# Kernel optimization log

Hardware: AMD Instinct MI355X
Metric: run time of the kernel (lower is better)

Reference implementation:

```python
import jax, jax.numpy as jnp
import numpy as np

B, S, H = 2, 2048, 2048
E, I, SH = 8, 768, 5632
TOP_K = 2


def setup_inputs() -> dict:
    key = jax.random.key(0)
    ks = jax.random.split(key, 8)
    sc = lambda *shape: 1.0 / np.sqrt(shape[-2] if len(shape) > 1 else 1.0)
    return {
        "hidden_states": jax.random.normal(ks[0], (B, S, H), jnp.float32),
        "router_w": jax.random.normal(ks[1], (H, E), jnp.float32) * (1.0 / np.sqrt(H)),
        "expert_gate_up_w": jax.random.normal(ks[2], (E, H, 2 * I), jnp.float32) * (1.0 / np.sqrt(H)),
        "expert_down_w": jax.random.normal(ks[3], (E, I, H), jnp.float32) * (1.0 / np.sqrt(I)),
        "shared_gate_w": jax.random.normal(ks[4], (H, SH), jnp.float32) * (1.0 / np.sqrt(H)),
        "shared_up_w": jax.random.normal(ks[5], (H, SH), jnp.float32) * (1.0 / np.sqrt(H)),
        "shared_down_w": jax.random.normal(ks[6], (SH, H), jnp.float32) * (1.0 / np.sqrt(SH)),
        "shared_expert_gate_w": jax.random.normal(ks[7], (H, 1), jnp.float32) * (1.0 / np.sqrt(H)),
    }


def reference(hidden_states, router_w, expert_gate_up_w, expert_down_w,
              shared_gate_w, shared_up_w, shared_down_w, shared_expert_gate_w):
    b, s, h = hidden_states.shape
    x = hidden_states.reshape(-1, h)  # [T, H]

    # Shared expert (SwiGLU) gated by sigmoid scalar gate per token.
    gate = jax.nn.silu((x @ shared_gate_w).astype(jnp.float32)).astype(x.dtype)
    shared_out = (gate * (x @ shared_up_w)) @ shared_down_w  # [T, H]
    shared_out = jax.nn.sigmoid(x @ shared_expert_gate_w) * shared_out

    # Router: softmax -> top-k -> renormalize -> dense routing weights [E, T].
    router_logits = x @ router_w  # [T, E]
    router_probs = jax.nn.softmax(router_logits, axis=-1)
    top_p, top_i = jax.lax.top_k(router_probs, TOP_K)  # [T, k]
    top_p = top_p / jnp.sum(top_p, axis=-1, keepdims=True)
    one_hot = jax.nn.one_hot(top_i, E, dtype=top_p.dtype)  # [T, k, E]
    routing_full = jnp.sum(one_hot * top_p[..., None], axis=1)  # [T, E]
    routing_full = routing_full.T.astype(x.dtype)  # [E, T]

    # Dense per-expert SwiGLU over all tokens (as in source einsums).
    gate_up = jnp.einsum('th,ehm->etm', x, expert_gate_up_w)  # [E, T, 2I]
    g, u = jnp.split(gate_up, 2, axis=-1)
    g = jax.nn.silu(g.astype(jnp.float32)).astype(x.dtype)
    expert_out = jnp.einsum('eti,eih->eth', u * g, expert_down_w)  # [E, T, H]

    expert_contribution = jnp.sum(expert_out * routing_full[:, :, None], axis=0)  # [T, H]
    out = (expert_contribution + shared_out).reshape(b, s, h)
    return out, router_logits
```

## Files before the change

### kernel.cpp

```cpp
#include <hip/hip_runtime.h>
#include <hip/hip_bf16.h>
#include <stdint.h>

#define DEVFN static __device__ __forceinline__

typedef __attribute__((ext_vector_type(8))) short bf16x8;
typedef __attribute__((ext_vector_type(4))) float f32x4;
typedef unsigned short u16;
typedef unsigned int u32;
typedef unsigned long long u64;

DEVFN u16 f2bf(float f) {
    union { float f; u32 u; } v; v.f = f;
    u32 r = v.u + 0x7FFFu + ((v.u >> 16) & 1u);
    return (u16)(r >> 16);
}

DEVFN void g2l16(const void* g, void* l) {
    __builtin_amdgcn_global_load_lds(
        (const __attribute__((address_space(1))) u32*)g,
        (__attribute__((address_space(3))) u32*)l, 16, 0, 0);
}

DEVFN void hbar() {
    __asm__ __volatile__("" ::: "memory");
    __builtin_amdgcn_s_barrier();
    __asm__ __volatile__("" ::: "memory");
}
DEVFN void vm4() { asm volatile("s_waitcnt vmcnt(4)" ::: "memory"); }
DEVFN void vm0() { asm volatile("s_waitcnt vmcnt(0)" ::: "memory"); }

__global__ __launch_bounds__(512, 2) void gemm8_swiglu_k(
    const u16* __restrict__ A, const u16* __restrict__ Bg,
    const u16* __restrict__ Bu, u16* __restrict__ out,
    int K, int nx, int ldc)
{
    extern __shared__ char smraw[];
    char* smA = smraw;
    char* smB = smraw + 65536;

    const int tid = threadIdx.x;
    const int lane = tid & 63, wv = tid >> 6;
    const int wm = wv >> 2, wn = wv & 3;
    const int l15 = lane & 15, kg = lane >> 4;

    const int nwg = gridDim.x;
    const int id = (blockIdx.x & 7) * (nwg >> 3) + (blockIdx.x >> 3);
    const int m0 = (id / nx) * 256, n0 = (id % nx) * 128;

    const u16* Ap  = A  + (long)m0 * K;
    const u16* Bgp = Bg + (long)n0 * K;
    const u16* Bup = Bu + (long)n0 * K;

    f32x4 accg[8][2], accu[8][2];
#pragma unroll
    for (int i = 0; i < 8; ++i)
#pragma unroll
        for (int j = 0; j < 2; ++j) {
            accg[i][j] = f32x4{0.f, 0.f, 0.f, 0.f};
            accu[i][j] = f32x4{0.f, 0.f, 0.f, 0.f};
        }

    auto stA = [&](int kt, int hh, int buf) {
        const u16* src = Ap + ((long)hh * 128) * K + kt * 64;
        char* dst = smA + buf * 32768 + hh * 16384;
#pragma unroll
        for (int i = 0; i < 2; ++i) {
            int slot = i * 512 + tid;
            int row = slot >> 3, ch = slot & 7;
            g2l16(src + (long)row * K + ((ch ^ (row & 7)) << 3), dst + slot * 16);
        }
    };
    auto stB = [&](int kt, int hh, int buf) {
        const u16* src = (hh ? Bup : Bgp) + kt * 64;
        char* dst = smB + buf * 32768 + hh * 16384;
#pragma unroll
        for (int i = 0; i < 2; ++i) {
            int slot = i * 512 + tid;
            int row = slot >> 3, ch = slot & 7;
            g2l16(src + (long)row * K + ((ch ^ (row & 7)) << 3), dst + slot * 16);
        }
    };
    auto frag = [&](const char* base, int r, int c) -> bf16x8 {
        return *(const __attribute__((address_space(3))) bf16x8*)
            (base + r * 128 + ((c ^ (r & 7)) << 4));
    };

    stA(0, 0, 0); stA(0, 1, 0);
    stB(0, 0, 0); stB(0, 1, 0);
    stB(1, 0, 1); stB(1, 1, 1);
    vm4();
    hbar();

    const int nk = K >> 6;
    for (int kt = 0; kt < nk; kt += 2) {
        const bool more = (kt + 2) < nk;
#pragma unroll
        for (int h = 0; h < 2; ++h) {
            const char* ab = smA + h * 32768;
            const char* bb = smB + h * 32768;
            bf16x8 bgv[2][2], buv[2][2];
#pragma unroll
            for (int p = 0; p < 4; ++p) {
                if (p == 0) {
#pragma unroll
                    for (int fn = 0; fn < 2; ++fn)
#pragma unroll
                        for (int s = 0; s < 2; ++s) {
                            int rB = wn * 32 + fn * 16 + l15;
                            bgv[fn][s] = frag(bb, rB, s * 4 + kg);
                            buv[fn][s] = frag(bb + 16384, rB, s * 4 + kg);
                        }
                }
                bf16x8 av[2][2];
#pragma unroll
                for (int am = 0; am < 2; ++am)
#pragma unroll
                    for (int s = 0; s < 2; ++s)
                        av[am][s] = frag(ab, wm * 128 + (p * 2 + am) * 16 + l15,
                                         s * 4 + kg);
                if (h == 0) {
                    if (p == 0)      { stA(kt + 1, 0, 1); stA(kt + 1, 1, 1); }
                    else if (p == 1) { if (more) stB(kt + 2, 0, 0); }
                    else if (p == 2) { if (more) stB(kt + 2, 1, 0); }
                    else             { if (more) vm4(); else vm0(); }
                } else {
                    if (more) {
                        if (p == 0)      stA(kt + 2, 0, 0);
                        else if (p == 1) stA(kt + 2, 1, 0);
                        else if (p == 2) stB(kt + 3, 0, 1);
                        else             { stB(kt + 3, 1, 1); vm4(); }
                    }
                }
                hbar();
                __builtin_amdgcn_sched_barrier(0);
                __builtin_amdgcn_s_setprio(1);
#pragma unroll
                for (int am = 0; am < 2; ++am)
#pragma unroll
                    for (int s = 0; s < 2; ++s)
#pragma unroll
                        for (int fn = 0; fn < 2; ++fn) {
                            accg[p * 2 + am][fn] = __builtin_amdgcn_mfma_f32_16x16x32_bf16(
                                av[am][s], bgv[fn][s], accg[p * 2 + am][fn], 0, 0, 0);
                            accu[p * 2 + am][fn] = __builtin_amdgcn_mfma_f32_16x16x32_bf16(
                                av[am][s], buv[fn][s], accu[p * 2 + am][fn], 0, 0, 0);
                        }
                __builtin_amdgcn_s_setprio(0);
                __builtin_amdgcn_sched_barrier(0);
                hbar();
            }
        }
    }

    const int lq = lane >> 4;
#pragma unroll
    for (int fm = 0; fm < 8; ++fm)
#pragma unroll
        for (int j = 0; j < 4; ++j) {
            int row = m0 + wm * 128 + fm * 16 + lq * 4 + j;
#pragma unroll
            for (int fn = 0; fn < 2; ++fn) {
                int col = n0 + wn * 32 + fn * 16 + l15;
                float g = accg[fm][fn][j], u = accu[fm][fn][j];
                float s = g * (1.f / (1.f + __expf(-g))) * u;
                out[(long)row * ldc + col] = f2bf(s);
            }
        }
}

template<int NSLOT>
DEVFN void stage(const u16* __restrict__ src, int ldk, u16* lds, int tid) {
#pragma unroll
    for (int i = 0; i < NSLOT / 256; ++i) {
        int slot = i * 256 + tid;
        int row = slot >> 2, chunk = slot & 3;
        int kg = chunk ^ ((row >> 1) & 3);
        g2l16(src + (long)row * ldk + kg * 8, lds + slot * 8);
    }
}

DEVFN bf16x8 ld_frag(const u16* lds, int row, int kg) {
    int chunk = kg ^ ((row >> 1) & 3);
    const u16* p = lds + row * 32 + chunk * 8;
    return *(const __attribute__((address_space(3))) bf16x8*)p;
}

__global__ __launch_bounds__(256) void gemm_down_k(
    const u16* __restrict__ A, const u16* __restrict__ B,
    float* __restrict__ C, const float* __restrict__ gvec,
    int K, int ldc)
{
    __shared__ u16 sm[2][8192];
    const int tid = threadIdx.x;
    const int lane = tid & 63, wv = tid >> 6;
    const int wm = wv >> 1, wn = wv & 1;
    const int m0 = blockIdx.y * 128, n0 = blockIdx.x * 128;
    const u16* Ab = A + (long)m0 * K;
    const u16* Bb = B + (long)n0 * K;

    f32x4 acc[4][4];
#pragma unroll
    for (int i = 0; i < 4; ++i)
#pragma unroll
        for (int j = 0; j < 4; ++j) acc[i][j] = f32x4{0.f, 0.f, 0.f, 0.f};

    stage<512>(Ab, K, &sm[0][0], tid);
    stage<512>(Bb, K, &sm[0][4096], tid);

    const int nk = K >> 5;
    for (int kt = 0; kt < nk; ++kt) {
        const int cur = kt & 1;
        __syncthreads();
        if (kt + 1 < nk) {
            stage<512>(Ab + (kt + 1) * 32, K, &sm[cur ^ 1][0], tid);
            stage<512>(Bb + (kt + 1) * 32, K, &sm[cur ^ 1][4096], tid);
        }
        const int l15 = lane & 15, kg = lane >> 4;
        bf16x8 av[4], bv[4];
#pragma unroll
        for (int f = 0; f < 4; ++f) {
            av[f] = ld_frag(&sm[cur][0],    wm * 64 + f * 16 + l15, kg);
            bv[f] = ld_frag(&sm[cur][4096], wn * 64 + f * 16 + l15, kg);
        }
#pragma unroll
        for (int fm = 0; fm < 4; ++fm)
#pragma unroll
            for (int fn = 0; fn < 4; ++fn)
                acc[fm][fn] = __builtin_amdgcn_mfma_f32_16x16x32_bf16(
                    av[fm], bv[fn], acc[fm][fn], 0, 0, 0);
    }

    const int l15 = lane & 15, lq = lane >> 4;
#pragma unroll
    for (int fm = 0; fm < 4; ++fm) {
#pragma unroll
        for (int j = 0; j < 4; ++j) {
            int row = m0 + wm * 64 + fm * 16 + lq * 4 + j;
            float gmul = gvec[row];
#pragma unroll
            for (int fn = 0; fn < 4; ++fn) {
                int col = n0 + wn * 64 + fn * 16 + l15;
                C[(long)row * ldc + col] = acc[fm][fn][j] * gmul;
            }
        }
    }
}

__global__ __launch_bounds__(256) void gemm_swiglu_moe_k(
    const u16* __restrict__ xb, const u16* __restrict__ Beg,
    const u16* __restrict__ Beu, const int* __restrict__ tok,
    const int* __restrict__ cntp, u16* __restrict__ eact,
    int K, int I_, int cap)
{
    const int e = blockIdx.z;
    const int m0 = blockIdx.y * 128;
    if (m0 >= cntp[e]) return;
    const int n0 = blockIdx.x * 64;

    __shared__ u16 sm[2][8192];
    const int tid = threadIdx.x;
    const int lane = tid & 63, wv = tid >> 6;
    const int wm = wv >> 1, wn = wv & 1;

    const int rA0 = tid >> 2, rA1 = 64 + (tid >> 2);
    const int* tseg = tok + (long)e * cap + m0;
    const long t0 = tseg[rA0], t1 = tseg[rA1];
    const int kg0 = (tid & 3) ^ ((rA0 >> 1) & 3);
    const int kg1 = (tid & 3) ^ ((rA1 >> 1) & 3);
    const u16* pa0 = xb + t0 * K + kg0 * 8;
    const u16* pa1 = xb + t1 * K + kg1 * 8;

    const u16* Bgb = Beg + ((long)e * I_ + n0) * K;
    const u16* Bub = Beu + ((long)e * I_ + n0) * K;

    f32x4 ag[4][2], au[4][2];
#pragma unroll
    for (int i = 0; i < 4; ++i)
#pragma unroll
        for (int j = 0; j < 2; ++j) {
            ag[i][j] = f32x4{0.f, 0.f, 0.f, 0.f};
            au[i][j] = f32x4{0.f, 0.f, 0.f, 0.f};
        }

    g2l16(pa0, &sm[0][(long)tid * 8]);
    g2l16(pa1, &sm[0][(long)(256 + tid) * 8]);
    stage<256>(Bgb, K, &sm[0][4096], tid);
    stage<256>(Bub, K, &sm[0][6144], tid);

    const int nk = K >> 5;
    for (int kt = 0; kt < nk; ++kt) {
        const int cur = kt & 1;
        __syncthreads();
        if (kt + 1 < nk) {
            g2l16(pa0 + (kt + 1) * 32, &sm[cur ^ 1][(long)tid * 8]);
            g2l16(pa1 + (kt + 1) * 32, &sm[cur ^ 1][(long)(256 + tid) * 8]);
            stage<256>(Bgb + (kt + 1) * 32, K, &sm[cur ^ 1][4096], tid);
            stage<256>(Bub + (kt + 1) * 32, K, &sm[cur ^ 1][6144], tid);
        }
        const int l15 = lane & 15, kg = lane >> 4;
        bf16x8 av[4], gv[2], uv[2];
#pragma unroll
        for (int f = 0; f < 4; ++f)
            av[f] = ld_frag(&sm[cur][0], wm * 64 + f * 16 + l15, kg);
#pragma unroll
        for (int f = 0; f < 2; ++f) {
            gv[f] = ld_frag(&sm[cur][4096], wn * 32 + f * 16 + l15, kg);
            uv[f] = ld_frag(&sm[cur][6144], wn * 32 + f * 16 + l15, kg);
        }
#pragma unroll
        for (int fm = 0; fm < 4; ++fm)
#pragma unroll
            for (int fn = 0; fn < 2; ++fn) {
                ag[fm][fn] = __builtin_amdgcn_mfma_f32_16x16x32_bf16(
                    av[fm], gv[fn], ag[fm][fn], 0, 0, 0);
                au[fm][fn] = __builtin_amdgcn_mfma_f32_16x16x32_bf16(
                    av[fm], uv[fn], au[fm][fn], 0, 0, 0);
            }
    }

    const int l15 = lane & 15, lq = lane >> 4;
#pragma unroll
    for (int fm = 0; fm < 4; ++fm) {
#pragma unroll
        for (int j = 0; j < 4; ++j) {
            long row = (long)e * cap + m0 + wm * 64 + fm * 16 + lq * 4 + j;
#pragma unroll
            for (int fn = 0; fn < 2; ++fn) {
                int col = n0 + wn * 32 + fn * 16 + l15;
                float g = ag[fm][fn][j], u = au[fm][fn][j];
                float s = g * (1.f / (1.f + __expf(-g))) * u;
                eact[row * I_ + col] = f2bf(s);
            }
        }
    }
}

__global__ __launch_bounds__(256) void gemm_down_moe_k(
    const u16* __restrict__ eact, const u16* __restrict__ Bed,
    float* __restrict__ out, const int* __restrict__ tok,
    const float* __restrict__ wrow, const int* __restrict__ cntp,
    int K, int ldc, int cap)
{
    const int e = blockIdx.z;
    const int m0 = blockIdx.y * 128;
    if (m0 >= cntp[e]) return;
    const int n0 = blockIdx.x * 128;

    __shared__ u16 sm[2][8192];
    const int tid = threadIdx.x;
    const int lane = tid & 63, wv = tid >> 6;
    const int wm = wv >> 1, wn = wv & 1;
    const u16* Ab = eact + ((long)e * cap + m0) * K;
    const u16* Bb = Bed + (long)e * ldc * K + (long)n0 * K;

    f32x4 acc[4][4];
#pragma unroll
    for (int i = 0; i < 4; ++i)
#pragma unroll
        for (int j = 0; j < 4; ++j) acc[i][j] = f32x4{0.f, 0.f, 0.f, 0.f};

    stage<512>(Ab, K, &sm[0][0], tid);
    stage<512>(Bb, K, &sm[0][4096], tid);

    const int nk = K >> 5;
    for (int kt = 0; kt < nk; ++kt) {
        const int cur = kt & 1;
        __syncthreads();
        if (kt + 1 < nk) {
            stage<512>(Ab + (kt + 1) * 32, K, &sm[cur ^ 1][0], tid);
            stage<512>(Bb + (kt + 1) * 32, K, &sm[cur ^ 1][4096], tid);
        }
        const int l15 = lane & 15, kg = lane >> 4;
        bf16x8 av[4], bv[4];
#pragma unroll
        for (int f = 0; f < 4; ++f) {
            av[f] = ld_frag(&sm[cur][0],    wm * 64 + f * 16 + l15, kg);
            bv[f] = ld_frag(&sm[cur][4096], wn * 64 + f * 16 + l15, kg);
        }
#pragma unroll
        for (int fm = 0; fm < 4; ++fm)
#pragma unroll
            for (int fn = 0; fn < 4; ++fn)
                acc[fm][fn] = __builtin_amdgcn_mfma_f32_16x16x32_bf16(
                    av[fm], bv[fn], acc[fm][fn], 0, 0, 0);
    }

    const int l15 = lane & 15, lq = lane >> 4;
#pragma unroll
    for (int fm = 0; fm < 4; ++fm) {
#pragma unroll
        for (int j = 0; j < 4; ++j) {
            long crow = (long)e * cap + m0 + wm * 64 + fm * 16 + lq * 4 + j;
            float w = wrow[crow];
            if (w != 0.f) {
                long t = tok[crow];
#pragma unroll
                for (int fn = 0; fn < 4; ++fn) {
                    int col = n0 + wn * 64 + fn * 16 + l15;
                    atomicAdd(out + t * ldc + col, acc[fm][fn][j] * w);
                }
            }
        }
    }
}

__global__ __launch_bounds__(256) void router_k(
    const float* __restrict__ x, const float* __restrict__ rw,
    const float* __restrict__ sgw, float* __restrict__ logits,
    int2* __restrict__ te, float2* __restrict__ tw,
    float* __restrict__ sig, int T, int H)
{
    const int tid = threadIdx.x, lane = tid & 63, wv = tid >> 6;
    const int t = blockIdx.x * 4 + wv;
    const float* xr = x + (long)t * H;
    float acc[8] = {0, 0, 0, 0, 0, 0, 0, 0};
    float as = 0.f;
    for (int h = lane; h < H; h += 64) {
        float xv = xr[h];
        const float* r = rw + h * 8;
#pragma unroll
        for (int e = 0; e < 8; ++e) acc[e] += xv * r[e];
        as += xv * sgw[h];
    }
#pragma unroll
    for (int off = 32; off; off >>= 1) {
#pragma unroll
        for (int e = 0; e < 8; ++e) acc[e] += __shfl_xor(acc[e], off);
        as += __shfl_xor(as, off);
    }
    if (lane == 0) {
        float mx = acc[0];
#pragma unroll
        for (int e = 1; e < 8; ++e) mx = fmaxf(mx, acc[e]);
        float p[8], sum = 0.f;
#pragma unroll
        for (int e = 0; e < 8; ++e) { p[e] = expf(acc[e] - mx); sum += p[e]; }
        int i1 = 0;
#pragma unroll
        for (int e = 1; e < 8; ++e) if (p[e] > p[i1]) i1 = e;
        int i2 = (i1 == 0) ? 1 : 0;
#pragma unroll
        for (int e = 0; e < 8; ++e) if (e != i1 && p[e] > p[i2]) i2 = e;
        float den = p[i1] + p[i2];
        te[t] = make_int2(i1, i2);
        tw[t] = make_float2(p[i1] / den, p[i2] / den);
#pragma unroll
        for (int e = 0; e < 8; ++e) logits[(long)t * 8 + e] = acc[e];
        sig[t] = 1.f / (1.f + expf(-as));
    }
}

__global__ __launch_bounds__(256) void compact_k(
    const int2* __restrict__ te, const float2* __restrict__ tw,
    int* __restrict__ tok, float* __restrict__ wrow,
    int* __restrict__ cntp, int T, int cap)
{
    const int e = blockIdx.x;
    const int tid = threadIdx.x, lane = tid & 63, wv = tid >> 6;
    __shared__ int wtot[4];
    int cnt = 0;
    for (int c0 = 0; c0 < T; c0 += 256) {
        int t = c0 + tid;
        int2 ids = te[t];
        float2 ws = tw[t];
        float w = (ids.x == e) ? ws.x : ((ids.y == e) ? ws.y : -1.f);
        bool sel = (w >= 0.f);
        u64 b = __ballot(sel);
        int rln = __popcll(b & ((1ull << lane) - 1ull));
        if (lane == 0) wtot[wv] = __popcll(b);
        __syncthreads();
        int rank = rln, tot = 0;
#pragma unroll
        for (int k = 0; k < 4; ++k) { if (k < wv) rank += wtot[k]; tot += wtot[k]; }
        if (sel) {
            int pos = cnt + rank;
            if (pos < cap) {
                tok[(long)e * cap + pos] = t;
                wrow[(long)e * cap + pos] = w;
            }
        }
        cnt += tot;
        __syncthreads();
    }
    if (cnt > cap) cnt = cap;
    int cp = (cnt + 127) & ~127;
    for (int p = cnt + tid; p < cp; p += 256) {
        tok[(long)e * cap + p] = 0;
        wrow[(long)e * cap + p] = 0.f;
    }
    if (tid == 0) cntp[e] = cp;
}

__global__ __launch_bounds__(256) void transpose_k(
    const float* __restrict__ src0, long src_zstr, int src_ld,
    u16* __restrict__ dst0, long dst_zstr, int dst_ld)
{
    __shared__ float tile[32][33];
    const float* src = src0 + (long)blockIdx.z * src_zstr;
    u16* dst = dst0 + (long)blockIdx.z * dst_zstr;
    int r0 = blockIdx.y * 32, c0 = blockIdx.x * 32;
    int tx = threadIdx.x, ty = threadIdx.y;
#pragma unroll
    for (int k = 0; k < 4; ++k)
        tile[ty + 8 * k][tx] = src[(long)(r0 + ty + 8 * k) * src_ld + c0 + tx];
    __syncthreads();
#pragma unroll
    for (int k = 0; k < 4; ++k)
        dst[(long)(c0 + ty + 8 * k) * dst_ld + r0 + tx] = f2bf(tile[tx][ty + 8 * k]);
}

__global__ __launch_bounds__(256) void cvt_x_k(const float* __restrict__ x,
                                               u16* __restrict__ xb)
{
    long i = ((long)blockIdx.x * 256 + threadIdx.x) * 4;
    float4 v = *(const float4*)(x + i);
    union { u16 s[4]; uint2 v2; } o;
    o.s[0] = f2bf(v.x); o.s[1] = f2bf(v.y); o.s[2] = f2bf(v.z); o.s[3] = f2bf(v.w);
    *(uint2*)(xb + i) = o.v2;
}

extern "C" void kernel_launch(void* const* d_in, const int* in_sizes, int n_in,
                              void* d_out, int out_size, void* d_ws, size_t ws_size,
                              hipStream_t stream) {
    (void)in_sizes; (void)n_in; (void)out_size; (void)ws_size;
    const int Hd = 2048, E = 8, I = 768, SH = 5632, T = 4096, CAP = 2048;

    const float* x    = (const float*)d_in[0];
    const float* rw   = (const float*)d_in[1];
    const float* egu  = (const float*)d_in[2];
    const float* edw  = (const float*)d_in[3];
    const float* sgw  = (const float*)d_in[4];
    const float* suw  = (const float*)d_in[5];
    const float* sdw  = (const float*)d_in[6];
    const float* segw = (const float*)d_in[7];
    float* out = (float*)d_out;
    float* logits = out + (size_t)T * Hd;

    char* wsp = (char*)d_ws;
    size_t off = 0;
    auto alloc = [&](size_t bytes) {
        void* p = wsp + off; off += (bytes + 255) & ~(size_t)255; return p;
    };
    u16* xb   = (u16*)alloc((size_t)T * Hd * 2);
    u16* Bgs  = (u16*)alloc((size_t)SH * Hd * 2);
    u16* Bus  = (u16*)alloc((size_t)SH * Hd * 2);
    u16* Bds  = (u16*)alloc((size_t)Hd * SH * 2);
    u16* Beg  = (u16*)alloc((size_t)E * I * Hd * 2);
    u16* Beu  = (u16*)alloc((size_t)E * I * Hd * 2);
    u16* Bed  = (u16*)alloc((size_t)E * Hd * I * 2);
    u16* hs   = (u16*)alloc((size_t)T * SH * 2);
    u16* eact = (u16*)alloc((size_t)E * CAP * I * 2);
    int2*   te   = (int2*)alloc((size_t)T * 8);
    float2* tw   = (float2*)alloc((size_t)T * 8);
    int*    tok  = (int*)alloc((size_t)E * CAP * 4);
    float*  wrow = (float*)alloc((size_t)E * CAP * 4);
    int*    cntp = (int*)alloc(64);
    float*  sig  = (float*)alloc((size_t)T * 4);

    hipFuncSetAttribute((const void*)gemm8_swiglu_k,
                        hipFuncAttributeMaxDynamicSharedMemorySize, 131072);

    dim3 tb(32, 8);
    cvt_x_k<<<(T * Hd) / 1024, 256, 0, stream>>>(x, xb);
    router_k<<<T / 4, 256, 0, stream>>>(x, rw, segw, logits, te, tw, sig, T, Hd);
    compact_k<<<E, 256, 0, stream>>>(te, tw, tok, wrow, cntp, T, CAP);

    transpose_k<<<dim3(SH / 32, Hd / 32), tb, 0, stream>>>(sgw, 0, SH, Bgs, 0, Hd);
    transpose_k<<<dim3(SH / 32, Hd / 32), tb, 0, stream>>>(suw, 0, SH, Bus, 0, Hd);
    transpose_k<<<dim3(Hd / 32, SH / 32), tb, 0, stream>>>(sdw, 0, Hd, Bds, 0, SH);
    transpose_k<<<dim3(I / 32, Hd / 32, E), tb, 0, stream>>>(
        egu, (long)Hd * 2 * I, 2 * I, Beg, (long)I * Hd, Hd);
    transpose_k<<<dim3(I / 32, Hd / 32, E), tb, 0, stream>>>(
        egu + I, (long)Hd * 2 * I, 2 * I, Beu, (long)I * Hd, Hd);
    transpose_k<<<dim3(Hd / 32, I / 32, E), tb, 0, stream>>>(
        edw, (long)I * Hd, Hd, Bed, (long)Hd * I, I);

    gemm8_swiglu_k<<<dim3((SH / 128) * (T / 256)), 512, 131072, stream>>>(
        xb, Bgs, Bus, hs, Hd, SH / 128, SH);
    gemm_down_k<<<dim3(Hd / 128, T / 128), 256, 0, stream>>>(
        hs, Bds, out, sig, SH, Hd);
    gemm_swiglu_moe_k<<<dim3(I / 64, CAP / 128, E), 256, 0, stream>>>(
        xb, Beg, Beu, tok, cntp, eact, Hd, I, CAP);
    gemm_down_moe_k<<<dim3(Hd / 128, CAP / 128, E), 256, 0, stream>>>(
        eact, Bed, out, tok, wrow, cntp, I, Hd, CAP);
}
```

Before: 612.3 us.

## Software-pipeline LDS fragment reads in shared GEMM and add 8-wave down GEMM

The shared-expert gate/up GEMM's main loop now runs as 8 phases. Each phase prefetches the next phase's A/B fragments from LDS into double-buffered registers while the MFMAs for the current phase run, with one barrier per phase instead of two, and global-to-LDS loads are interleaved with relaxed vmcnt waits. The shared down-projection GEMM is replaced by a new 512-thread, 256x128-tile kernel that uses the same pipelined scheme, replacing the 256-thread 128x128 kernel with single-stage 32-wide K steps. The aim is to hide LDS latency and cut barrier overhead, at the cost of more registers and a tricky wait/barrier ordering that could race if miscounted.

```diff
diff --git a/kernel.cpp b/kernel.cpp
--- a/kernel.cpp
+++ b/kernel.cpp
@@ -22,13 +22,17 @@
         (__attribute__((address_space(3))) u32*)l, 16, 0, 0);
 }
 
-DEVFN void hbar() {
-    __asm__ __volatile__("" ::: "memory");
+DEVFN void vmw0() { asm volatile("s_waitcnt vmcnt(0)" ::: "memory"); }
+DEVFN void vmw2() { asm volatile("s_waitcnt vmcnt(2)" ::: "memory"); }
+DEVFN void vmw4() { asm volatile("s_waitcnt vmcnt(4)" ::: "memory"); }
+DEVFN void vmw6() { asm volatile("s_waitcnt vmcnt(6)" ::: "memory"); }
+DEVFN void vmw8() { asm volatile("s_waitcnt vmcnt(8)" ::: "memory"); }
+DEVFN void pbar() {
+    __builtin_amdgcn_sched_barrier(0);
     __builtin_amdgcn_s_barrier();
-    __asm__ __volatile__("" ::: "memory");
-}
-DEVFN void vm4() { asm volatile("s_waitcnt vmcnt(4)" ::: "memory"); }
-DEVFN void vm0() { asm volatile("s_waitcnt vmcnt(0)" ::: "memory"); }
+}
+
+#define MFMA16(a, b, c) __builtin_amdgcn_mfma_f32_16x16x32_bf16(a, b, c, 0, 0, 0)
 
 __global__ __launch_bounds__(512, 2) void gemm8_swiglu_k(
     const u16* __restrict__ A, const u16* __restrict__ Bg,
@@ -86,70 +90,67 @@
             (base + r * 128 + ((c ^ (r & 7)) << 4));
     };
 
-    stA(0, 0, 0); stA(0, 1, 0);
-    stB(0, 0, 0); stB(0, 1, 0);
-    stB(1, 0, 1); stB(1, 1, 1);
-    vm4();
-    hbar();
+    bf16x8 af[2][4];
+    bf16x8 bgf[2][2], buf2[2][2];
+
+    auto rdA = [&](int par, int h, int s, int fmh) {
+#pragma unroll
+        for (int i = 0; i < 4; ++i)
+            af[par][i] = frag(smA + h * 32768,
+                              wm * 128 + fmh * 64 + i * 16 + l15, s * 4 + kg);
+    };
+    auto rdB = [&](int set, int h, int s) {
+#pragma unroll
+        for (int fn = 0; fn < 2; ++fn) {
+            bgf[set][fn] = frag(smB + h * 32768,
+                                wn * 32 + fn * 16 + l15, s * 4 + kg);
+            buf2[set][fn] = frag(smB + h * 32768 + 16384,
+                                 wn * 32 + fn * 16 + l15, s * 4 + kg);
+        }
+    };
+
+    stA(0, 0, 0); stA(0, 1, 0); stB(0, 0, 0); stB(0, 1, 0);
+    stA(1, 0, 1); stA(1, 1, 1); stB(1, 0, 1); stB(1, 1, 1);
+    vmw8();
+    __builtin_amdgcn_s_barrier();
+    rdA(0, 0, 0, 0);
+    rdB(0, 0, 0);
 
     const int nk = K >> 6;
     for (int kt = 0; kt < nk; kt += 2) {
         const bool more = (kt + 2) < nk;
 #pragma unroll
-        for (int h = 0; h < 2; ++h) {
-            const char* ab = smA + h * 32768;
-            const char* bb = smB + h * 32768;
-            bf16x8 bgv[2][2], buv[2][2];
-#pragma unroll
-            for (int p = 0; p < 4; ++p) {
-                if (p == 0) {
-#pragma unroll
-                    for (int fn = 0; fn < 2; ++fn)
-#pragma unroll
-                        for (int s = 0; s < 2; ++s) {
-                            int rB = wn * 32 + fn * 16 + l15;
-                            bgv[fn][s] = frag(bb, rB, s * 4 + kg);
-                            buv[fn][s] = frag(bb + 16384, rB, s * 4 + kg);
-                        }
+        for (int p = 0; p < 8; ++p) {
+            if (p < 7) {
+                const int tp = p + 1;
+                rdA(tp & 1, tp >> 2, (tp >> 1) & 1, tp & 1);
+                if ((tp & 1) == 0) rdB((tp >> 1) & 1, tp >> 2, (tp >> 1) & 1);
+            } else if (more) {
+                rdA(0, 0, 0, 0);
+                rdB(0, 0, 0);
+            }
+            if (more) {
+                if (p == 3)      stB(kt + 2, 0, 0);
+                else if (p == 4) { stB(kt + 2, 1, 0); stA(kt + 2, 0, 0); }
+                else if (p == 5) stA(kt + 2, 1, 0);
+                else if (p == 6) stB(kt + 3, 0, 1);
+                else if (p == 7) { stB(kt + 3, 1, 1); stA(kt + 3, 0, 1); stA(kt + 3, 1, 1); }
+            }
+            if (p == 2) vmw0();
+            if (p == 6 && more) vmw2();
+            pbar();
+            __builtin_amdgcn_s_setprio(1);
+            const int fb = p & 1, sb = (p >> 1) & 1;
+#pragma unroll
+            for (int i = 0; i < 4; ++i)
+#pragma unroll
+                for (int fn = 0; fn < 2; ++fn) {
+                    accg[fb * 4 + i][fn] = MFMA16(af[fb][i], bgf[sb][fn],
+                                                  accg[fb * 4 + i][fn]);
+                    accu[fb * 4 + i][fn] = MFMA16(af[fb][i], buf2[sb][fn],
+                                                  accu[fb * 4 + i][fn]);
                 }
-                bf16x8 av[2][2];
-#pragma unroll
-                for (int am = 0; am < 2; ++am)
-#pragma unroll
-                    for (int s = 0; s < 2; ++s)
-                        av[am][s] = frag(ab, wm * 128 + (p * 2 + am) * 16 + l15,
-                                         s * 4 + kg);
-                if (h == 0) {
-                    if (p == 0)      { stA(kt + 1, 0, 1); stA(kt + 1, 1, 1); }
-                    else if (p == 1) { if (more) stB(kt + 2, 0, 0); }
-                    else if (p == 2) { if (more) stB(kt + 2, 1, 0); }
-                    else             { if (more) vm4(); else vm0(); }
-                } else {
-                    if (more) {
-                        if (p == 0)      stA(kt + 2, 0, 0);
-                        else if (p == 1) stA(kt + 2, 1, 0);
-                        else if (p == 2) stB(kt + 3, 0, 1);
-                        else             { stB(kt + 3, 1, 1); vm4(); }
-                    }
-                }
-                hbar();
-                __builtin_amdgcn_sched_barrier(0);
-                __builtin_amdgcn_s_setprio(1);
-#pragma unroll
-                for (int am = 0; am < 2; ++am)
-#pragma unroll
-                    for (int s = 0; s < 2; ++s)
-#pragma unroll
-                        for (int fn = 0; fn < 2; ++fn) {
-                            accg[p * 2 + am][fn] = __builtin_amdgcn_mfma_f32_16x16x32_bf16(
-                                av[am][s], bgv[fn][s], accg[p * 2 + am][fn], 0, 0, 0);
-                            accu[p * 2 + am][fn] = __builtin_amdgcn_mfma_f32_16x16x32_bf16(
-                                av[am][s], buv[fn][s], accu[p * 2 + am][fn], 0, 0, 0);
-                        }
-                __builtin_amdgcn_s_setprio(0);
-                __builtin_amdgcn_sched_barrier(0);
-                hbar();
-            }
+            __builtin_amdgcn_s_setprio(0);
         }
     }
 
@@ -169,6 +170,130 @@
         }
 }
 
+__global__ __launch_bounds__(512, 2) void gemm8_down_k(
+    const u16* __restrict__ A, const u16* __restrict__ B,
+    float* __restrict__ C, const float* __restrict__ gvec,
+    int K, int nx, int ldc)
+{
+    extern __shared__ char smraw[];
+    char* smA = smraw;
+    char* smB = smraw + 65536;
+
+    const int tid = threadIdx.x;
+    const int lane = tid & 63, wv = tid >> 6;
+    const int wm = wv >> 2, wn = wv & 3;
+    const int l15 = lane & 15, kg = lane >> 4;
+
+    const int nwg = gridDim.x;
+    const int id = (blockIdx.x & 7) * (nwg >> 3) + (blockIdx.x >> 3);
+    const int m0 = (id / nx) * 256, n0 = (id % nx) * 128;
+
+    const u16* Ap = A + (long)m0 * K;
+    const u16* Bp = B + (long)n0 * K;
+
+    f32x4 acc[8][2];
+#pragma unroll
+    for (int i = 0; i < 8; ++i)
+#pragma unroll
+        for (int j = 0; j < 2; ++j) acc[i][j] = f32x4{0.f, 0.f, 0.f, 0.f};
+
+    auto stA = [&](int kt, int hh, int buf) {
+        const u16* src = Ap + ((long)hh * 128) * K + kt * 64;
+        char* dst = smA + buf * 32768 + hh * 16384;
+#pragma unroll
+        for (int i = 0; i < 2; ++i) {
+            int slot = i * 512 + tid;
+            int row = slot >> 3, ch = slot & 7;
+            g2l16(src + (long)row * K + ((ch ^ (row & 7)) << 3), dst + slot * 16);
+        }
+    };
+    auto stB1 = [&](int kt, int buf) {
+        const u16* src = Bp + kt * 64;
+        char* dst = smB + buf * 16384;
+#pragma unroll
+        for (int i = 0; i < 2; ++i) {
+            int slot = i * 512 + tid;
+            int row = slot >> 3, ch = slot & 7;
+            g2l16(src + (long)row * K + ((ch ^ (row & 7)) << 3), dst + slot * 16);
+        }
+    };
+    auto frag = [&](const char* base, int r, int c) -> bf16x8 {
+        return *(const __attribute__((address_space(3))) bf16x8*)
+            (base + r * 128 + ((c ^ (r & 7)) << 4));
+    };
+
+    bf16x8 af[2][4], bf_[2][2];
+
+    auto rdA = [&](int par, int h, int s, int fmh) {
+#pragma unroll
+        for (int i = 0; i < 4; ++i)
+            af[par][i] = frag(smA + h * 32768,
+                              wm * 128 + fmh * 64 + i * 16 + l15, s * 4 + kg);
+    };
+    auto rdB = [&](int set, int h, int s) {
+#pragma unroll
+        for (int fn = 0; fn < 2; ++fn)
+            bf_[set][fn] = frag(smB + h * 16384,
+                                wn * 32 + fn * 16 + l15, s * 4 + kg);
+    };
+
+    stA(0, 0, 0); stA(0, 1, 0); stB1(0, 0);
+    stA(1, 0, 1); stA(1, 1, 1); stB1(1, 1);
+    vmw6();
+    __builtin_amdgcn_s_barrier();
+    rdA(0, 0, 0, 0);
+    rdB(0, 0, 0);
+
+    const int nk = K >> 6;
+    for (int kt = 0; kt < nk; kt += 2) {
+        const bool more = (kt + 2) < nk;
+#pragma unroll
+        for (int p = 0; p < 8; ++p) {
+            if (p < 7) {
+                const int tp = p + 1;
+                rdA(tp & 1, tp >> 2, (tp >> 1) & 1, tp & 1);
+                if ((tp & 1) == 0) rdB((tp >> 1) & 1, tp >> 2, (tp >> 1) & 1);
+            } else if (more) {
+                rdA(0, 0, 0, 0);
+                rdB(0, 0, 0);
+            }
+            if (more) {
+                if (p == 3)      stB1(kt + 2, 0);
+                else if (p == 4) stA(kt + 2, 0, 0);
+                else if (p == 5) stA(kt + 2, 1, 0);
+                else if (p == 6) stB1(kt + 3, 1);
+                else if (p == 7) { stA(kt + 3, 0, 1); stA(kt + 3, 1, 1); }
+            }
+            if (p == 2) vmw0();
+            if (p == 6 && more) vmw2();
+            pbar();
+            __builtin_amdgcn_s_setprio(1);
+            const int fb = p & 1, sb = (p >> 1) & 1;
+#pragma unroll
+            for (int i = 0; i < 4; ++i)
+#pragma unroll
+                for (int fn = 0; fn < 2; ++fn)
+                    acc[fb * 4 + i][fn] = MFMA16(af[fb][i], bf_[sb][fn],
+                                                 acc[fb * 4 + i][fn]);
+            __builtin_amdgcn_s_setprio(0);
+        }
+    }
+
+    const int lq = lane >> 4;
+#pragma unroll
+    for (int fm = 0; fm < 8; ++fm)
+#pragma unroll
+        for (int j = 0; j < 4; ++j) {
+            int row = m0 + wm * 128 + fm * 16 + lq * 4 + j;
+            float gmul = gvec[row];
+#pragma unroll
+            for (int fn = 0; fn < 2; ++fn) {
+                int col = n0 + wn * 32 + fn * 16 + l15;
+                C[(long)row * ldc + col] = acc[fm][fn][j] * gmul;
+            }
+        }
+}
+
 template<int NSLOT>
 DEVFN void stage(const u16* __restrict__ src, int ldk, u16* lds, int tid) {
 #pragma unroll
@@ -184,67 +309,6 @@
     int chunk = kg ^ ((row >> 1) & 3);
     const u16* p = lds + row * 32 + chunk * 8;
     return *(const __attribute__((address_space(3))) bf16x8*)p;
-}
-
-__global__ __launch_bounds__(256) void gemm_down_k(
-    const u16* __restrict__ A, const u16* __restrict__ B,
-    float* __restrict__ C, const float* __restrict__ gvec,
-    int K, int ldc)
-{
-    __shared__ u16 sm[2][8192];
-    const int tid = threadIdx.x;
-    const int lane = tid & 63, wv = tid >> 6;
-    const int wm = wv >> 1, wn = wv & 1;
-    const int m0 = blockIdx.y * 128, n0 = blockIdx.x * 128;
-    const u16* Ab = A + (long)m0 * K;
-    const u16* Bb = B + (long)n0 * K;
-
-    f32x4 acc[4][4];
-#pragma unroll
-    for (int i = 0; i < 4; ++i)
-#pragma unroll
-        for (int j = 0; j < 4; ++j) acc[i][j] = f32x4{0.f, 0.f, 0.f, 0.f};
-
-    stage<512>(Ab, K, &sm[0][0], tid);
-    stage<512>(Bb, K, &sm[0][4096], tid);
-
-    const int nk = K >> 5;
-    for (int kt = 0; kt < nk; ++kt) {
-        const int cur = kt & 1;
-        __syncthreads();
-        if (kt + 1 < nk) {
-            stage<512>(Ab + (kt + 1) * 32, K, &sm[cur ^ 1][0], tid);
-            stage<512>(Bb + (kt + 1) * 32, K, &sm[cur ^ 1][4096], tid);
-        }
-        const int l15 = lane & 15, kg = lane >> 4;
-        bf16x8 av[4], bv[4];
-#pragma unroll
-        for (int f = 0; f < 4; ++f) {
-            av[f] = ld_frag(&sm[cur][0],    wm * 64 + f * 16 + l15, kg);
-            bv[f] = ld_frag(&sm[cur][4096], wn * 64 + f * 16 + l15, kg);
-        }
-#pragma unroll
-        for (int fm = 0; fm < 4; ++fm)
-#pragma unroll
-            for (int fn = 0; fn < 4; ++fn)
-                acc[fm][fn] = __builtin_amdgcn_mfma_f32_16x16x32_bf16(
-                    av[fm], bv[fn], acc[fm][fn], 0, 0, 0);
-    }
-
-    const int l15 = lane & 15, lq = lane >> 4;
-#pragma unroll
-    for (int fm = 0; fm < 4; ++fm) {
-#pragma unroll
-        for (int j = 0; j < 4; ++j) {
-            int row = m0 + wm * 64 + fm * 16 + lq * 4 + j;
-            float gmul = gvec[row];
-#pragma unroll
-            for (int fn = 0; fn < 4; ++fn) {
-                int col = n0 + wn * 64 + fn * 16 + l15;
-                C[(long)row * ldc + col] = acc[fm][fn][j] * gmul;
-            }
-        }
-    }
 }
 
 __global__ __launch_bounds__(256) void gemm_swiglu_moe_k(
@@ -312,10 +376,8 @@
         for (int fm = 0; fm < 4; ++fm)
 #pragma unroll
             for (int fn = 0; fn < 2; ++fn) {
-                ag[fm][fn] = __builtin_amdgcn_mfma_f32_16x16x32_bf16(
-                    av[fm], gv[fn], ag[fm][fn], 0, 0, 0);
-                au[fm][fn] = __builtin_amdgcn_mfma_f32_16x16x32_bf16(
-                    av[fm], uv[fn], au[fm][fn], 0, 0, 0);
+                ag[fm][fn] = MFMA16(av[fm], gv[fn], ag[fm][fn]);
+                au[fm][fn] = MFMA16(av[fm], uv[fn], au[fm][fn]);
             }
     }
 
@@ -382,8 +444,7 @@
         for (int fm = 0; fm < 4; ++fm)
 #pragma unroll
             for (int fn = 0; fn < 4; ++fn)
-                acc[fm][fn] = __builtin_amdgcn_mfma_f32_16x16x32_bf16(
-                    av[fm], bv[fn], acc[fm][fn], 0, 0, 0);
+                acc[fm][fn] = MFMA16(av[fm], bv[fn], acc[fm][fn]);
     }
 
     const int l15 = lane & 15, lq = lane >> 4;
@@ -560,6 +621,8 @@
 
     hipFuncSetAttribute((const void*)gemm8_swiglu_k,
                         hipFuncAttributeMaxDynamicSharedMemorySize, 131072);
+    hipFuncSetAttribute((const void*)gemm8_down_k,
+                        hipFuncAttributeMaxDynamicSharedMemorySize, 98304);
 
     dim3 tb(32, 8);
     cvt_x_k<<<(T * Hd) / 1024, 256, 0, stream>>>(x, xb);
@@ -578,8 +641,8 @@
 
     gemm8_swiglu_k<<<dim3((SH / 128) * (T / 256)), 512, 131072, stream>>>(
         xb, Bgs, Bus, hs, Hd, SH / 128, SH);
-    gemm_down_k<<<dim3(Hd / 128, T / 128), 256, 0, stream>>>(
-        hs, Bds, out, sig, SH, Hd);
+    gemm8_down_k<<<dim3((Hd / 128) * (T / 256)), 512, 98304, stream>>>(
+        hs, Bds, out, sig, SH, Hd / 128, Hd);
     gemm_swiglu_moe_k<<<dim3(I / 64, CAP / 128, E), 256, 0, stream>>>(
         xb, Beg, Beu, tok, cntp, eact, Hd, I, CAP);
     gemm_down_moe_k<<<dim3(Hd / 128, CAP / 128, E), 256, 0, stream>>>(
```

New measurement: 1.169 ms. 90.9% more time.

## Port routed-expert gate/up GEMM to the 256x128 pipelined 8-wave kernel

Applied to the files above, without the earlier changes.

Replaces the simple double-buffered 128x64 MoE gate/up kernel with a version of the shared-expert 512-thread kernel. It uses 256x128 tiles, gathered token rows, a multi-stage global-to-LDS pipeline and fused SwiGLU. Per-expert token counts are now padded to multiples of 256, capped at capacity, so the larger tiles line up with the padding. The intent is more data reuse per tile and better overlap of loads with MFMA work. The cost is more padded rows per expert and fewer blocks in flight.

```diff
diff --git a/kernel.cpp b/kernel.cpp
--- a/kernel.cpp
+++ b/kernel.cpp
@@ -30,6 +30,8 @@
 DEVFN void vm4() { asm volatile("s_waitcnt vmcnt(4)" ::: "memory"); }
 DEVFN void vm0() { asm volatile("s_waitcnt vmcnt(0)" ::: "memory"); }
 
+#define MFMA16(a, b, c) __builtin_amdgcn_mfma_f32_16x16x32_bf16(a, b, c, 0, 0, 0)
+
 __global__ __launch_bounds__(512, 2) void gemm8_swiglu_k(
     const u16* __restrict__ A, const u16* __restrict__ Bg,
     const u16* __restrict__ Bu, u16* __restrict__ out,
@@ -83,7 +85,7 @@
     };
     auto frag = [&](const char* base, int r, int c) -> bf16x8 {
         return *(const __attribute__((address_space(3))) bf16x8*)
-            (base + r * 128 + ((c ^ (r & 7)) << 4));
+            (base + r * 128 + (((c) ^ (r & 7)) << 4));
     };
 
     stA(0, 0, 0); stA(0, 1, 0);
@@ -141,10 +143,10 @@
                     for (int s = 0; s < 2; ++s)
 #pragma unroll
                         for (int fn = 0; fn < 2; ++fn) {
-                            accg[p * 2 + am][fn] = __builtin_amdgcn_mfma_f32_16x16x32_bf16(
-                                av[am][s], bgv[fn][s], accg[p * 2 + am][fn], 0, 0, 0);
-                            accu[p * 2 + am][fn] = __builtin_amdgcn_mfma_f32_16x16x32_bf16(
-                                av[am][s], buv[fn][s], accu[p * 2 + am][fn], 0, 0, 0);
+                            accg[p * 2 + am][fn] = MFMA16(av[am][s], bgv[fn][s],
+                                                          accg[p * 2 + am][fn]);
+                            accu[p * 2 + am][fn] = MFMA16(av[am][s], buv[fn][s],
+                                                          accu[p * 2 + am][fn]);
                         }
                 __builtin_amdgcn_s_setprio(0);
                 __builtin_amdgcn_sched_barrier(0);
@@ -165,6 +167,151 @@
                 float g = accg[fm][fn][j], u = accu[fm][fn][j];
                 float s = g * (1.f / (1.f + __expf(-g))) * u;
                 out[(long)row * ldc + col] = f2bf(s);
+            }
+        }
+}
+
+__global__ __launch_bounds__(512, 2) void gemm8e_swiglu_k(
+    const u16* __restrict__ xb, const u16* __restrict__ Beg,
+    const u16* __restrict__ Beu, const int* __restrict__ tok,
+    const int* __restrict__ cntp, u16* __restrict__ eact,
+    int K, int ldc, int cap)
+{
+    const int e = blockIdx.z;
+    const int m0 = blockIdx.y * 256;
+    if (m0 >= cntp[e]) return;
+    const int n0 = blockIdx.x * 128;
+
+    extern __shared__ char smraw[];
+    char* smA = smraw;
+    char* smB = smraw + 65536;
+
+    const int tid = threadIdx.x;
+    const int lane = tid & 63, wv = tid >> 6;
+    const int wm = wv >> 2, wn = wv & 3;
+    const int l15 = lane & 15, kg = lane >> 4;
+
+    const int r0 = tid >> 3, ch = tid & 7;
+    const int swz = (ch ^ (r0 & 7)) << 3;
+    const int* tseg = tok + (long)e * cap + m0;
+    const u16* pa00 = xb + (long)tseg[r0] * K + swz;
+    const u16* pa01 = xb + (long)tseg[64 + r0] * K + swz;
+    const u16* pa10 = xb + (long)tseg[128 + r0] * K + swz;
+    const u16* pa11 = xb + (long)tseg[192 + r0] * K + swz;
+
+    const u16* Bgp = Beg + ((long)e * ldc + n0) * K;
+    const u16* Bup = Beu + ((long)e * ldc + n0) * K;
+
+    f32x4 accg[8][2], accu[8][2];
+#pragma unroll
+    for (int i = 0; i < 8; ++i)
+#pragma unroll
+        for (int j = 0; j < 2; ++j) {
+            accg[i][j] = f32x4{0.f, 0.f, 0.f, 0.f};
+            accu[i][j] = f32x4{0.f, 0.f, 0.f, 0.f};
+        }
+
+    auto stA = [&](int kt, int hh, int buf) {
+        char* dst = smA + buf * 32768 + hh * 16384;
+        const u16* p0 = hh ? pa10 : pa00;
+        const u16* p1 = hh ? pa11 : pa01;
+        g2l16(p0 + kt * 64, dst + (long)tid * 16);
+        g2l16(p1 + kt * 64, dst + (long)(512 + tid) * 16);
+    };
+    auto stB = [&](int kt, int hh, int buf) {
+        const u16* src = (hh ? Bup : Bgp) + kt * 64;
+        char* dst = smB + buf * 32768 + hh * 16384;
+#pragma unroll
+        for (int i = 0; i < 2; ++i) {
+            int slot = i * 512 + tid;
+            int row = slot >> 3, c = slot & 7;
+            g2l16(src + (long)row * K + ((c ^ (row & 7)) << 3), dst + slot * 16);
+        }
+    };
+    auto frag = [&](const char* base, int r, int c) -> bf16x8 {
+        return *(const __attribute__((address_space(3))) bf16x8*)
+            (base + r * 128 + (((c) ^ (r & 7)) << 4));
+    };
+
+    stA(0, 0, 0); stA(0, 1, 0);
+    stB(0, 0, 0); stB(0, 1, 0);
+    stB(1, 0, 1); stB(1, 1, 1);
+    vm4();
+    hbar();
+
+    const int nk = K >> 6;
+    for (int kt = 0; kt < nk; kt += 2) {
+        const bool more = (kt + 2) < nk;
+#pragma unroll
+        for (int h = 0; h < 2; ++h) {
+            const char* ab = smA + h * 32768;
+            const char* bb = smB + h * 32768;
+            bf16x8 bgv[2][2], buv[2][2];
+#pragma unroll
+            for (int p = 0; p < 4; ++p) {
+                if (p == 0) {
+#pragma unroll
+                    for (int fn = 0; fn < 2; ++fn)
+#pragma unroll
+                        for (int s = 0; s < 2; ++s) {
+                            int rB = wn * 32 + fn * 16 + l15;
+                            bgv[fn][s] = frag(bb, rB, s * 4 + kg);
+                            buv[fn][s] = frag(bb + 16384, rB, s * 4 + kg);
+                        }
+                }
+                bf16x8 av[2][2];
+#pragma unroll
+                for (int am = 0; am < 2; ++am)
+#pragma unroll
+                    for (int s = 0; s < 2; ++s)
+                        av[am][s] = frag(ab, wm * 128 + (p * 2 + am) * 16 + l15,
+                                         s * 4 + kg);
+                if (h == 0) {
+                    if (p == 0)      { stA(kt + 1, 0, 1); stA(kt + 1, 1, 1); }
+                    else if (p == 1) { if (more) stB(kt + 2, 0, 0); }
+                    else if (p == 2) { if (more) stB(kt + 2, 1, 0); }
+                    else             { if (more) vm4(); else vm0(); }
+                } else {
+                    if (more) {
+                        if (p == 0)      stA(kt + 2, 0, 0);
+                        else if (p == 1) stA(kt + 2, 1, 0);
+                        else if (p == 2) stB(kt + 3, 0, 1);
+                        else             { stB(kt + 3, 1, 1); vm4(); }
+                    }
+                }
+                hbar();
+                __builtin_amdgcn_sched_barrier(0);
+                __builtin_amdgcn_s_setprio(1);
+#pragma unroll
+                for (int am = 0; am < 2; ++am)
+#pragma unroll
+                    for (int s = 0; s < 2; ++s)
+#pragma unroll
+                        for (int fn = 0; fn < 2; ++fn) {
+                            accg[p * 2 + am][fn] = MFMA16(av[am][s], bgv[fn][s],
+                                                          accg[p * 2 + am][fn]);
+                            accu[p * 2 + am][fn] = MFMA16(av[am][s], buv[fn][s],
+                                                          accu[p * 2 + am][fn]);
+                        }
+                __builtin_amdgcn_s_setprio(0);
+                __builtin_amdgcn_sched_barrier(0);
+                hbar();
+            }
+        }
+    }
+
+    const int lq = lane >> 4;
+#pragma unroll
+    for (int fm = 0; fm < 8; ++fm)
+#pragma unroll
+        for (int j = 0; j < 4; ++j) {
+            long row = (long)e * cap + m0 + wm * 128 + fm * 16 + lq * 4 + j;
+#pragma unroll
+            for (int fn = 0; fn < 2; ++fn) {
+                int col = n0 + wn * 32 + fn * 16 + l15;
+                float g = accg[fm][fn][j], u = accu[fm][fn][j];
+                float s = g * (1.f / (1.f + __expf(-g))) * u;
+                eact[row * ldc + col] = f2bf(s);
             }
         }
 }
@@ -227,8 +374,7 @@
         for (int fm = 0; fm < 4; ++fm)
 #pragma unroll
             for (int fn = 0; fn < 4; ++fn)
-                acc[fm][fn] = __builtin_amdgcn_mfma_f32_16x16x32_bf16(
-                    av[fm], bv[fn], acc[fm][fn], 0, 0, 0);
+                acc[fm][fn] = MFMA16(av[fm], bv[fn], acc[fm][fn]);
     }
 
     const int l15 = lane & 15, lq = lane >> 4;
@@ -242,95 +388,6 @@
             for (int fn = 0; fn < 4; ++fn) {
                 int col = n0 + wn * 64 + fn * 16 + l15;
                 C[(long)row * ldc + col] = acc[fm][fn][j] * gmul;
-            }
-        }
-    }
-}
-
-__global__ __launch_bounds__(256) void gemm_swiglu_moe_k(
-    const u16* __restrict__ xb, const u16* __restrict__ Beg,
-    const u16* __restrict__ Beu, const int* __restrict__ tok,
-    const int* __restrict__ cntp, u16* __restrict__ eact,
-    int K, int I_, int cap)
-{
-    const int e = blockIdx.z;
-    const int m0 = blockIdx.y * 128;
-    if (m0 >= cntp[e]) return;
-    const int n0 = blockIdx.x * 64;
-
-    __shared__ u16 sm[2][8192];
-    const int tid = threadIdx.x;
-    const int lane = tid & 63, wv = tid >> 6;
-    const int wm = wv >> 1, wn = wv & 1;
-
-    const int rA0 = tid >> 2, rA1 = 64 + (tid >> 2);
-    const int* tseg = tok + (long)e * cap + m0;
-    const long t0 = tseg[rA0], t1 = tseg[rA1];
-    const int kg0 = (tid & 3) ^ ((rA0 >> 1) & 3);
-    const int kg1 = (tid & 3) ^ ((rA1 >> 1) & 3);
-    const u16* pa0 = xb + t0 * K + kg0 * 8;
-    const u16* pa1 = xb + t1 * K + kg1 * 8;
-
-    const u16* Bgb = Beg + ((long)e * I_ + n0) * K;
-    const u16* Bub = Beu + ((long)e * I_ + n0) * K;
-
-    f32x4 ag[4][2], au[4][2];
-#pragma unroll
-    for (int i = 0; i < 4; ++i)
-#pragma unroll
-        for (int j = 0; j < 2; ++j) {
-            ag[i][j] = f32x4{0.f, 0.f, 0.f, 0.f};
-            au[i][j] = f32x4{0.f, 0.f, 0.f, 0.f};
-        }
-
-    g2l16(pa0, &sm[0][(long)tid * 8]);
-    g2l16(pa1, &sm[0][(long)(256 + tid) * 8]);
-    stage<256>(Bgb, K, &sm[0][4096], tid);
-    stage<256>(Bub, K, &sm[0][6144], tid);
-
-    const int nk = K >> 5;
-    for (int kt = 0; kt < nk; ++kt) {
-        const int cur = kt & 1;
-        __syncthreads();
-        if (kt + 1 < nk) {
-            g2l16(pa0 + (kt + 1) * 32, &sm[cur ^ 1][(long)tid * 8]);
-            g2l16(pa1 + (kt + 1) * 32, &sm[cur ^ 1][(long)(256 + tid) * 8]);
-            stage<256>(Bgb + (kt + 1) * 32, K, &sm[cur ^ 1][4096], tid);
-            stage<256>(Bub + (kt + 1) * 32, K, &sm[cur ^ 1][6144], tid);
-        }
-        const int l15 = lane & 15, kg = lane >> 4;
-        bf16x8 av[4], gv[2], uv[2];
-#pragma unroll
-        for (int f = 0; f < 4; ++f)
-            av[f] = ld_frag(&sm[cur][0], wm * 64 + f * 16 + l15, kg);
-#pragma unroll
-        for (int f = 0; f < 2; ++f) {
-            gv[f] = ld_frag(&sm[cur][4096], wn * 32 + f * 16 + l15, kg);
-            uv[f] = ld_frag(&sm[cur][6144], wn * 32 + f * 16 + l15, kg);
-        }
-#pragma unroll
-        for (int fm = 0; fm < 4; ++fm)
-#pragma unroll
-            for (int fn = 0; fn < 2; ++fn) {
-                ag[fm][fn] = __builtin_amdgcn_mfma_f32_16x16x32_bf16(
-                    av[fm], gv[fn], ag[fm][fn], 0, 0, 0);
-                au[fm][fn] = __builtin_amdgcn_mfma_f32_16x16x32_bf16(
-                    av[fm], uv[fn], au[fm][fn], 0, 0, 0);
-            }
-    }
-
-    const int l15 = lane & 15, lq = lane >> 4;
-#pragma unroll
-    for (int fm = 0; fm < 4; ++fm) {
-#pragma unroll
-        for (int j = 0; j < 4; ++j) {
-            long row = (long)e * cap + m0 + wm * 64 + fm * 16 + lq * 4 + j;
-#pragma unroll
-            for (int fn = 0; fn < 2; ++fn) {
-                int col = n0 + wn * 32 + fn * 16 + l15;
-                float g = ag[fm][fn][j], u = au[fm][fn][j];
-                float s = g * (1.f / (1.f + __expf(-g))) * u;
-                eact[row * I_ + col] = f2bf(s);
             }
         }
     }
@@ -382,8 +439,7 @@
         for (int fm = 0; fm < 4; ++fm)
 #pragma unroll
             for (int fn = 0; fn < 4; ++fn)
-                acc[fm][fn] = __builtin_amdgcn_mfma_f32_16x16x32_bf16(
-                    av[fm], bv[fn], acc[fm][fn], 0, 0, 0);
+                acc[fm][fn] = MFMA16(av[fm], bv[fn], acc[fm][fn]);
     }
 
     const int l15 = lane & 15, lq = lane >> 4;
@@ -484,7 +540,8 @@
         __syncthreads();
     }
     if (cnt > cap) cnt = cap;
-    int cp = (cnt + 127) & ~127;
+    int cp = (cnt + 255) & ~255;
+    if (cp > cap) cp = cap;
     for (int p = cnt + tid; p < cp; p += 256) {
         tok[(long)e * cap + p] = 0;
         wrow[(long)e * cap + p] = 0.f;
@@ -560,6 +617,8 @@
 
     hipFuncSetAttribute((const void*)gemm8_swiglu_k,
                         hipFuncAttributeMaxDynamicSharedMemorySize, 131072);
+    hipFuncSetAttribute((const void*)gemm8e_swiglu_k,
+                        hipFuncAttributeMaxDynamicSharedMemorySize, 131072);
 
     dim3 tb(32, 8);
     cvt_x_k<<<(T * Hd) / 1024, 256, 0, stream>>>(x, xb);
@@ -580,7 +639,7 @@
         xb, Bgs, Bus, hs, Hd, SH / 128, SH);
     gemm_down_k<<<dim3(Hd / 128, T / 128), 256, 0, stream>>>(
         hs, Bds, out, sig, SH, Hd);
-    gemm_swiglu_moe_k<<<dim3(I / 64, CAP / 128, E), 256, 0, stream>>>(
+    gemm8e_swiglu_k<<<dim3(I / 128, CAP / 256, E), 512, 131072, stream>>>(
         xb, Beg, Beu, tok, cntp, eact, Hd, I, CAP);
     gemm_down_moe_k<<<dim3(Hd / 128, CAP / 128, E), 256, 0, stream>>>(
         eact, Bed, out, tok, wrow, cntp, I, Hd, CAP);
```

New measurement: 578.6 us. 1.06x faster.
